# Performance work log

Hardware: AMD Instinct MI355X
Metric: run time of the kernel (lower is better)

Reference implementation:

```python
import jax, jax.numpy as jnp
import numpy as np

HISTORY = 64
WINDOW = 32
DIM = 32
N_PATTERNS = 16
AMP = 2.0


def setup_inputs() -> dict:
    key = jax.random.key(0)
    ks = jax.random.split(key, 7)
    B, L = 128, 131072
    T = L // WINDOW  # 4096 scan steps
    x = jax.random.normal(ks[0], (B, L), jnp.float32)
    avg = jax.random.normal(ks[1], (B, N_PATTERNS), jnp.float32)
    avg_scores = avg - avg.mean(axis=-1, keepdims=True)
    noise = jax.random.normal(ks[2], (B, T, WINDOW), jnp.float32)
    # keys: xavier_uniform on (dim, n_patterns)
    kbound = float(np.sqrt(6.0 / (DIM + N_PATTERNS)))
    keys = jax.random.uniform(ks[3], (DIM, N_PATTERNS), jnp.float32, -kbound, kbound)
    # shapes = rand(n_patterns, 2) * amp * 2
    shapes = jax.random.uniform(ks[4], (N_PATTERNS, 2), jnp.float32) * (AMP * 2.0)
    # conv1d default init: uniform(-1/sqrt(fan_in), 1/sqrt(fan_in)), fan_in = 1*history
    cb = float(1.0 / np.sqrt(HISTORY))
    conv_w = jax.random.uniform(ks[5], (DIM, 1, HISTORY), jnp.float32, -cb, cb)
    conv_b = jax.random.uniform(ks[6], (DIM,), jnp.float32, -cb, cb)
    return {"x": x, "avg_scores": avg_scores, "noise": noise,
            "conv_w": conv_w, "conv_b": conv_b, "keys": keys, "shapes": shapes}


def reference(x, avg_scores, noise, conv_w, conv_b, keys, shapes):
    B, L = x.shape
    inv_p = 1.0 / N_PATTERNS
    # left-pad by history-1, conv1d(1 -> dim, kernel=history, stride=window) + relu
    padded = jnp.pad(x, ((0, 0), (HISTORY - 1, 0)))[:, None, :]  # [B,1,L+H-1]
    out = jax.lax.conv_general_dilated(
        padded, conv_w, window_strides=(WINDOW,), padding='VALID',
        dimension_numbers=('NCH', 'OIH', 'NCH'))  # [B,dim,T]
    out = jax.nn.relu(out + conv_b[None, :, None])
    out = out.transpose(2, 0, 1)  # [T,B,dim]
    # relu6 attention scores against pattern keys
    attn_scores = jnp.clip(jnp.einsum('tbd,dp->tbp', out, keys), 0.0, 6.0)  # [T,B,P]

    def step(avg, score):
        prob = jax.nn.softmax(score - avg, axis=-1)  # [B,P]
        return avg + prob - inv_p, prob

    _, probs = jax.lax.scan(step, avg_scores, attn_scores)  # probs: [T,B,P]
    attn_probs = probs.transpose(1, 0, 2)  # [B,T,P]
    shapeparams = jnp.einsum('btp,pc->btc', attn_probs, shapes)  # [B,T,2]
    offset = shapeparams[:, :, 0:1]  # broadcast over window
    std = shapeparams[:, :, 1:2]
    signal = (offset + noise * std).reshape(B, -1)[:, :L]  # [B,L]
    return jax.nn.relu(signal - x)
```

## Files before the change

### kernel.cpp

```cpp
#include <hip/hip_runtime.h>

static constexpr int BATCH = 128;
static constexpr int LEN   = 131072;
static constexpr int T     = 4096;
static constexpr int DIM   = 32;
static constexpr int NP    = 16;

static constexpr int NCHUNK = 64;
static constexpr int SPC    = T / NCHUNK;
static constexpr int WARM   = 128;

static constexpr int TT = 128;

#define L2E   1.44269504088896340736f
#define L2E16 (1.44269504088896340736f / 16.0f)

typedef __attribute__((ext_vector_type(8))) short  short8;
typedef __attribute__((ext_vector_type(4))) float  f32x4;

__device__ __forceinline__ float fexp2(float x) {
#if __has_builtin(__builtin_amdgcn_exp2f)
  return __builtin_amdgcn_exp2f(x);
#else
  return exp2f(x);
#endif
}

__device__ __forceinline__ float frcp(float x) {
#if __has_builtin(__builtin_amdgcn_rcpf)
  return __builtin_amdgcn_rcpf(x);
#else
  return 1.0f / x;
#endif
}

template <int CTRL>
__device__ __forceinline__ float dppf(float v) {
  return __int_as_float(
      __builtin_amdgcn_update_dpp(0, __float_as_int(v), CTRL, 0xf, 0xf, true));
}

__device__ __forceinline__ float sum16(float v) {
  v += dppf<0xB1>(v);
  v += dppf<0x4E>(v);
  v += dppf<0x141>(v);
  v += dppf<0x140>(v);
  return v;
}

__device__ __forceinline__ short bf16c(float f) {
  unsigned u = __float_as_uint(f);
  unsigned r = u + 0x7fffu + ((u >> 16) & 1u);
  return (short)(r >> 16);
}

__global__ void __launch_bounds__(64) prep_kernel(
    const float* __restrict__ conv_w, const float* __restrict__ conv_b,
    const float* __restrict__ keys, short* __restrict__ frags) {
  int l = threadIdx.x;
  int ln15 = l & 15, kg = l >> 4;
#pragma unroll
  for (int fn = 0; fn < 2; ++fn)
#pragma unroll
    for (int fk = 0; fk < 2; ++fk) {
      const float* wp = conv_w + (fn * 16 + ln15) * 64 + fk * 32 + kg * 8;
      short* dst = frags + ((fn * 2 + fk) * 64 + l) * 8;
#pragma unroll
      for (int j = 0; j < 8; ++j) dst[j] = bf16c(wp[j]);
    }
  short* kd = frags + (256 + l) * 8;
#pragma unroll
  for (int j = 0; j < 8; ++j) kd[j] = bf16c(keys[(kg * 8 + j) * NP + ln15]);
  float* bp = (float*)(frags + 2560);
  bp[2 * l]     = conv_b[ln15];
  bp[2 * l + 1] = conv_b[16 + ln15];
}

__global__ void __launch_bounds__(256) scores_kernel(
    const float* __restrict__ x, const short* __restrict__ frags,
    _Float16* __restrict__ scoresh) {
  __shared__ short lds[4][1728];

  int tid = threadIdx.x;
  int lane = tid & 63;
  int mt   = tid >> 6;
  int blk = blockIdx.x;
  int b  = blk >> 5;
  int bt = blk & 31;
  int t0 = bt * TT;
  int T0w = t0 + mt * 32;
  const float* xb = x + (size_t)b * LEN;
  short* xw = lds[mt];
  short* rl = lds[mt] + 1088;

  int gbase = 32 * T0w - 64 + 16 * lane;
  float f[17];
#pragma unroll
  for (int s = 0; s < 4; ++s) {
    int gi = gbase + 4 * s;
    float4 v = make_float4(0.f, 0.f, 0.f, 0.f);
    if (gi >= 0) v = *(const float4*)(xb + gi);
    f[4 * s]     = v.x; f[4 * s + 1] = v.y;
    f[4 * s + 2] = v.z; f[4 * s + 3] = v.w;
  }
  f[16] = (gbase + 16 >= 0) ? xb[gbase + 16] : 0.f;

  short8 w0, w1;
#pragma unroll
  for (int j = 0; j < 8; ++j) { w0[j] = bf16c(f[j + 1]); w1[j] = bf16c(f[j + 9]); }
  *(short8*)(&xw[16 * lane])     = w0;
  *(short8*)(&xw[16 * lane + 8]) = w1;
  if (lane > 0) xw[16 * lane - 1] = bf16c(f[0]);
  if (lane < 32)
    xw[1024 + lane] = bf16c(xb[32 * T0w + 961 + lane]);

  int ln15 = lane & 15;
  int kg   = lane >> 4;

  const short8* wf = (const short8*)frags;
  short8 bw00 = wf[0 * 64 + lane];
  short8 bw01 = wf[1 * 64 + lane];
  short8 bw10 = wf[2 * 64 + lane];
  short8 bw11 = wf[3 * 64 + lane];
  short8 bk   = wf[4 * 64 + lane];
  const float2* bp = (const float2*)(frags + 2560);
  float2 bias = bp[lane];

  _Float16* dstb = scoresh + (b & 3) * 16 + ln15;

#pragma unroll
  for (int st = 0; st < 2; ++st) {
    int tl = st * 16 + ln15;
    const short* ap = &xw[32 * tl];
    short8 a0 = *(const short8*)(ap + kg * 8);
    short8 a1 = *(const short8*)(ap + 32 + kg * 8);

    f32x4 acc0 = {0.f, 0.f, 0.f, 0.f};
    f32x4 acc1 = {0.f, 0.f, 0.f, 0.f};
    acc0 = __builtin_amdgcn_mfma_f32_16x16x32_bf16(a0, bw00, acc0, 0, 0, 0);
    acc0 = __builtin_amdgcn_mfma_f32_16x16x32_bf16(a1, bw01, acc0, 0, 0, 0);
    acc1 = __builtin_amdgcn_mfma_f32_16x16x32_bf16(a0, bw10, acc1, 0, 0, 0);
    acc1 = __builtin_amdgcn_mfma_f32_16x16x32_bf16(a1, bw11, acc1, 0, 0, 0);

#pragma unroll
    for (int r = 0; r < 4; ++r) {
      int trow = kg * 4 + r;
      rl[trow * 40 + ln15]      = bf16c(fmaxf(acc0[r] + bias.x, 0.f));
      rl[trow * 40 + 16 + ln15] = bf16c(fmaxf(acc1[r] + bias.y, 0.f));
    }
    short8 a2 = *(const short8*)(&rl[ln15 * 40 + kg * 8]);
    f32x4 acc2 = {0.f, 0.f, 0.f, 0.f};
    acc2 = __builtin_amdgcn_mfma_f32_16x16x32_bf16(a2, bk, acc2, 0, 0, 0);

#pragma unroll
    for (int r = 0; r < 4; ++r) {
      float s = fminf(fmaxf(acc2[r], 0.f), 6.f) * L2E;
      int t = T0w + st * 16 + kg * 4 + r;
      dstb[((size_t)(b >> 2) * T + t) * 64] = (_Float16)s;
    }
  }
}

__global__ void __launch_bounds__(64) scan_kernel(
    const _Float16* __restrict__ scoresh, const float* __restrict__ avg0,
    const float* __restrict__ shapes, float2* __restrict__ osd) {
  int lane = threadIdx.x;
  int g = blockIdx.x & 31;
  int c = blockIdx.x >> 5;
  int gid = g * 64 + lane;
  int p = lane & 15;
  int bb = gid >> 4;
  float A = avg0[gid] * L2E;
  float sh0 = shapes[2 * p];
  float sh1 = shapes[2 * p + 1];
  int w = min(WARM, c * SPC);
  int tbeg = c * SPC - w;
  const _Float16* sp = scoresh + ((size_t)g * T + tbeg) * 64 + lane;

  float q0 = (float)sp[0 * 64],  q1 = (float)sp[1 * 64];
  float q2 = (float)sp[2 * 64],  q3 = (float)sp[3 * 64];
  float q4 = (float)sp[4 * 64],  q5 = (float)sp[5 * 64];
  float q6 = (float)sp[6 * 64],  q7 = (float)sp[7 * 64];
  float q8 = (float)sp[8 * 64],  q9 = (float)sp[9 * 64];
  float qa = (float)sp[10 * 64], qb = (float)sp[11 * 64];
  float qc = (float)sp[12 * 64], qd = (float)sp[13 * 64];
  float qe = (float)sp[14 * 64], qf = (float)sp[15 * 64];
  sp += 16 * 64;

#define WSTEP(Q)                                   \
  do {                                             \
    float e = fexp2(Q - A);                        \
    float r = sum16(e);                            \
    A = fmaf(e * L2E, frcp(r), A - L2E16);         \
    Q = (float)sp[0];                              \
    sp += 64;                                      \
  } while (0)

  for (int i = 0; i < w; i += 16) {
    WSTEP(q0); WSTEP(q1); WSTEP(q2); WSTEP(q3);
    WSTEP(q4); WSTEP(q5); WSTEP(q6); WSTEP(q7);
    WSTEP(q8); WSTEP(q9); WSTEP(qa); WSTEP(qb);
    WSTEP(qc); WSTEP(qd); WSTEP(qe); WSTEP(qf);
  }

  float2* od = osd + (size_t)bb * T + c * SPC;
#define CSTEP(Q, idx)                              \
  do {                                             \
    float e = fexp2(Q - A);                        \
    float r  = sum16(e);                           \
    float u0 = sum16(e * sh0);                     \
    float u1 = sum16(e * sh1);                     \
    float rc = frcp(r);                            \
    A = fmaf(e * L2E, rc, A - L2E16);              \
    if (p == 0) od[idx] = make_float2(u0 * rc, u1 * rc); \
    Q = (float)sp[0];                              \
    sp += 64;                                      \
  } while (0)

  for (int i = 0; i < SPC; i += 16) {
    CSTEP(q0, i + 0);  CSTEP(q1, i + 1);  CSTEP(q2, i + 2);  CSTEP(q3, i + 3);
    CSTEP(q4, i + 4);  CSTEP(q5, i + 5);  CSTEP(q6, i + 6);  CSTEP(q7, i + 7);
    CSTEP(q8, i + 8);  CSTEP(q9, i + 9);  CSTEP(qa, i + 10); CSTEP(qb, i + 11);
    CSTEP(qc, i + 12); CSTEP(qd, i + 13); CSTEP(qe, i + 14); CSTEP(qf, i + 15);
  }
#undef WSTEP
#undef CSTEP
}

__global__ void __launch_bounds__(256) out_kernel(
    const float* __restrict__ x, const float* __restrict__ noise,
    const float2* __restrict__ osd, float* __restrict__ out) {
  size_t gid = (size_t)blockIdx.x * 256 + threadIdx.x;
  size_t i4 = gid * 4;
  int b = (int)(i4 >> 17);
  int l = (int)(i4 & (LEN - 1));
  int t = l >> 5;
  float2 os = osd[(size_t)b * T + t];
  float4 xv = *(const float4*)(x + i4);
  float4 nv = *(const float4*)(noise + i4);
  float4 o;
  o.x = fmaxf(fmaf(nv.x, os.y, os.x) - xv.x, 0.f);
  o.y = fmaxf(fmaf(nv.y, os.y, os.x) - xv.y, 0.f);
  o.z = fmaxf(fmaf(nv.z, os.y, os.x) - xv.z, 0.f);
  o.w = fmaxf(fmaf(nv.w, os.y, os.x) - xv.w, 0.f);
  *(float4*)(out + i4) = o;
}

extern "C" void kernel_launch(void* const* d_in, const int* in_sizes, int n_in,
                              void* d_out, int out_size, void* d_ws, size_t ws_size,
                              hipStream_t stream) {
  const float* x      = (const float*)d_in[0];
  const float* avg0   = (const float*)d_in[1];
  const float* noise  = (const float*)d_in[2];
  const float* conv_w = (const float*)d_in[3];
  const float* conv_b = (const float*)d_in[4];
  const float* keys   = (const float*)d_in[5];
  const float* shapes = (const float*)d_in[6];
  float* out = (float*)d_out;

  _Float16* scoresh = (_Float16*)d_ws;
  char* p1 = (char*)d_ws + ((size_t)T * BATCH * NP * 2 + 4096);
  float2* osd = (float2*)p1;
  short* frags = (short*)(p1 + (size_t)BATCH * T * 8);

  prep_kernel<<<1, 64, 0, stream>>>(conv_w, conv_b, keys, frags);
  scores_kernel<<<BATCH * (T / TT), 256, 0, stream>>>(x, frags, scoresh);
  scan_kernel<<<32 * NCHUNK, 64, 0, stream>>>(scoresh, avg0, shapes, osd);
  out_kernel<<<(int)((size_t)BATCH * LEN / 4 / 256), 256, 0, stream>>>(x, noise, osd, out);
}
```

Baseline: 79.12 us.

## Fuse output elementwise pass into scan kernel via LDS-staged shape params

Merges the separate output kernel into the scan kernel. Each scan block writes its per-step offset and std values to shared memory, then streams the matching x and noise chunk (4 batches by 2048 elements) and writes the output. This drops the osd global round trip and one kernel launch. The cost is that the bandwidth-heavy elementwise pass now runs on only 2048 single-wave blocks, so it may get less memory-level parallelism than the old wide 256-thread launch.

New measurement: 71.17 us. 10.0% less time.

```diff
diff --git a/kernel.cpp b/kernel.cpp
--- a/kernel.cpp
+++ b/kernel.cpp
@@ -161,15 +161,18 @@
   }
 }
 
-__global__ void __launch_bounds__(64) scan_kernel(
+__global__ void __launch_bounds__(64) scanout_kernel(
     const _Float16* __restrict__ scoresh, const float* __restrict__ avg0,
-    const float* __restrict__ shapes, float2* __restrict__ osd) {
+    const float* __restrict__ shapes, const float* __restrict__ x,
+    const float* __restrict__ noise, float* __restrict__ out) {
+  __shared__ float2 oslds[4][64];
+
   int lane = threadIdx.x;
   int g = blockIdx.x & 31;
   int c = blockIdx.x >> 5;
   int gid = g * 64 + lane;
   int p = lane & 15;
-  int bb = gid >> 4;
+  int bl = lane >> 4;
   float A = avg0[gid] * L2E;
   float sh0 = shapes[2 * p];
   float sh1 = shapes[2 * p + 1];
@@ -203,7 +206,6 @@
     WSTEP(qc); WSTEP(qd); WSTEP(qe); WSTEP(qf);
   }
 
-  float2* od = osd + (size_t)bb * T + c * SPC;
 #define CSTEP(Q, idx)                              \
   do {                                             \
     float e = fexp2(Q - A);                        \
@@ -212,7 +214,7 @@
     float u1 = sum16(e * sh1);                     \
     float rc = frcp(r);                            \
     A = fmaf(e * L2E, rc, A - L2E16);              \
-    if (p == 0) od[idx] = make_float2(u0 * rc, u1 * rc); \
+    if (p == 0) oslds[bl][idx] = make_float2(u0 * rc, u1 * rc); \
     Q = (float)sp[0];                              \
     sp += 64;                                      \
   } while (0)
@@ -225,25 +227,30 @@
   }
 #undef WSTEP
 #undef CSTEP
-}
-
-__global__ void __launch_bounds__(256) out_kernel(
-    const float* __restrict__ x, const float* __restrict__ noise,
-    const float2* __restrict__ osd, float* __restrict__ out) {
-  size_t gid = (size_t)blockIdx.x * 256 + threadIdx.x;
-  size_t i4 = gid * 4;
-  int b = (int)(i4 >> 17);
-  int l = (int)(i4 & (LEN - 1));
-  int t = l >> 5;
-  float2 os = osd[(size_t)b * T + t];
-  float4 xv = *(const float4*)(x + i4);
-  float4 nv = *(const float4*)(noise + i4);
-  float4 o;
-  o.x = fmaxf(fmaf(nv.x, os.y, os.x) - xv.x, 0.f);
-  o.y = fmaxf(fmaf(nv.y, os.y, os.x) - xv.y, 0.f);
-  o.z = fmaxf(fmaf(nv.z, os.y, os.x) - xv.z, 0.f);
-  o.w = fmaxf(fmaf(nv.w, os.y, os.x) - xv.w, 0.f);
-  *(float4*)(out + i4) = o;
+
+  size_t base = (size_t)(g * 4) * LEN + (size_t)c * 2048;
+#pragma unroll
+  for (int bb = 0; bb < 4; ++bb) {
+    const float* xp = x     + base + (size_t)bb * LEN;
+    const float* np = noise + base + (size_t)bb * LEN;
+    float*       op = out   + base + (size_t)bb * LEN;
+    float4 xv[8], nv[8];
+#pragma unroll
+    for (int k = 0; k < 8; ++k) {
+      xv[k] = *(const float4*)(xp + (k * 64 + lane) * 4);
+      nv[k] = *(const float4*)(np + (k * 64 + lane) * 4);
+    }
+#pragma unroll
+    for (int k = 0; k < 8; ++k) {
+      float2 os = oslds[bb][k * 8 + (lane >> 3)];
+      float4 o;
+      o.x = fmaxf(fmaf(nv[k].x, os.y, os.x) - xv[k].x, 0.f);
+      o.y = fmaxf(fmaf(nv[k].y, os.y, os.x) - xv[k].y, 0.f);
+      o.z = fmaxf(fmaf(nv[k].z, os.y, os.x) - xv[k].z, 0.f);
+      o.w = fmaxf(fmaf(nv[k].w, os.y, os.x) - xv[k].w, 0.f);
+      *(float4*)(op + (k * 64 + lane) * 4) = o;
+    }
+  }
 }
 
 extern "C" void kernel_launch(void* const* d_in, const int* in_sizes, int n_in,
@@ -259,12 +266,9 @@
   float* out = (float*)d_out;
 
   _Float16* scoresh = (_Float16*)d_ws;
-  char* p1 = (char*)d_ws + ((size_t)T * BATCH * NP * 2 + 4096);
-  float2* osd = (float2*)p1;
-  short* frags = (short*)(p1 + (size_t)BATCH * T * 8);
+  short* frags = (short*)((char*)d_ws + ((size_t)T * BATCH * NP * 2 + 4096));
 
   prep_kernel<<<1, 64, 0, stream>>>(conv_w, conv_b, keys, frags);
   scores_kernel<<<BATCH * (T / TT), 256, 0, stream>>>(x, frags, scoresh);
-  scan_kernel<<<32 * NCHUNK, 64, 0, stream>>>(scoresh, avg0, shapes, osd);
-  out_kernel<<<(int)((size_t)BATCH * LEN / 4 / 256), 256, 0, stream>>>(x, noise, osd, out);
-}
+  scanout_kernel<<<32 * NCHUNK, 64, 0, stream>>>(scoresh, avg0, shapes, x, noise, out);
+}
```
